# Kernel optimization log

Hardware: AMD Instinct MI355X
Metric: run time of the kernel (lower is better)

## Reference

```python
import jax, jax.numpy as jnp
import numpy as np
from jax import lax

N, L, E, ED, H = 100000, 48, 1600000, 17, 48

def _lin_init(k, fan_in, fan_out):
    kw, kb = jax.random.split(k)
    s = 1.0 / np.sqrt(fan_in)
    W = jax.random.uniform(kw, (fan_in, fan_out), minval=-s, maxval=s, dtype=jnp.float32)
    b = jax.random.uniform(kb, (fan_out,), minval=-s, maxval=s, dtype=jnp.float32)
    return W, b

def setup_inputs() -> dict:
    key = jax.random.key(0)
    ks = jax.random.split(key, 10)
    nodes = jax.random.normal(ks[0], (N, L, 1), dtype=jnp.float32)
    edge_index = jax.random.randint(ks[1], (2, E), 0, N, dtype=jnp.int64) if jax.config.jax_enable_x64 else jax.random.randint(ks[1], (2, E), 0, N, dtype=jnp.int32)
    edge_attr = jax.random.normal(ks[2], (E, ED), dtype=jnp.float32)
    valid = (jax.random.uniform(ks[3], (1, N, L)) < 0.8).astype(jnp.float32)
    r = jnp.zeros((1,), jnp.float32)
    fx = jnp.zeros((1,), jnp.float32)
    W1, b1 = _lin_init(ks[4], ED, H)   # lin_edge[0]
    W2, b2 = _lin_init(ks[5], H, H)    # lin_edge[2]
    Wg, bg = _lin_init(ks[6], H, H)    # gru[0]
    Ww, bw = _lin_init(ks[7], H, 1)    # weight_mlp
    Wf, bf = _lin_init(ks[8], 3, 1)    # fuse_mlp
    return {"nodes": nodes, "edge_index": edge_index, "edge_attr": edge_attr,
            "valid": valid, "r": r, "fx": fx,
            "W1": W1, "b1": b1, "W2": W2, "b2": b2, "Wg": Wg, "bg": bg,
            "Ww": Ww, "bw": bw, "Wf": Wf, "bf": bf}

def _gelu(x):
    return jax.nn.gelu(x, approximate=False)  # torch GELU default is exact erf

def reference(nodes, edge_index, edge_attr, valid, r, fx,
              W1, b1, W2, b2, Wg, bg, Ww, bw, Wf, bf):
    n = nodes.shape[0]
    # torch.no_grad block: mask nodes by valid, flatten (C==1)
    v = lax.stop_gradient(valid[0][..., None])            # [N, L, 1]
    x = lax.stop_gradient((nodes * v).reshape(n, L))      # [N, L]
    original = x
    nv_mask = (1.0 - v).reshape(n, L)                     # not_valid mask [N, L]
    src, dst = edge_index[0], edge_index[1]
    for _ in range(3):
        # lin_edge: 17 -> 48 -> GELU -> 48 -> ReLU  (per edge)
        eh = jax.nn.relu(_gelu(edge_attr @ W1 + b1) @ W2 + b2)      # [E, 48]
        xc = jnp.concatenate([x, v[..., 0]], axis=-1)               # [N, 2L]
        x_j = xc[src]                                               # gather [E, 2L]
        g = _gelu(eh @ Wg + bg)                                     # gru
        w = g @ Ww + bw                                             # [E, 1]
        w = jnp.mean(x_j[:, L:], axis=-1, keepdims=True) * w
        msg = x_j * jax.nn.sigmoid(w)                               # [E, 2L]
        agg = jax.ops.segment_sum(msg, dst, num_segments=n)         # scatter-add [N, 2L]
        new_half = agg[:, :L]                                       # [N, L]
        nn3 = jnp.stack([new_half, x, nv_mask], axis=-1)            # [N, L, 3]
        mask = jax.nn.sigmoid((nn3 @ Wf + bf)[..., 0])              # [N, L]
        x = (1.0 - mask) * x + nv_mask * mask * new_half
        v = jnp.logical_or((original != x)[..., None], v > 0).astype(jnp.float32)
        v = v.at[:, 0].set(0.0)
        nv_mask = (1.0 - v).reshape(n, L)
    return x[0][None]  # [1, L]
```

## Files before the change

kernel.cpp:

```cpp
#include <hip/hip_runtime.h>
#include <math.h>

#define NN 100000
#define LF 48
#define NE 1600000
#define EDIMS 17
#define MASKW 3125
#define CAP_E 16384
#define MAXLOC 12288
#define EB 1563

static_assert(NN == MASKW * 32, "mask width");

__device__ __forceinline__ float gelu_f(float x) {
    return 0.5f * x * (1.0f + erff(x * 0.7071067811865475f));
}
__device__ __forceinline__ float sigm_f(float x) {
    return 1.0f / (1.0f + expf(-x));
}

__global__ void expand1_kernel(const int* __restrict__ src, const int* __restrict__ dst,
                               unsigned* __restrict__ M2, unsigned* __restrict__ M1,
                               unsigned* __restrict__ M0, float4* __restrict__ aggz,
                               int4* __restrict__ list0, int* __restrict__ counter)
{
    int tid = blockIdx.x * 256 + threadIdx.x;
    int nthr = (int)gridDim.x * 256;
    for (int i = tid; i < MASKW; i += nthr) { M1[i] = 0u; M0[i] = 0u; }
    for (int i = tid; i < (3 * MAXLOC * LF) / 4; i += nthr)
        aggz[i] = make_float4(0.f, 0.f, 0.f, 0.f);
    if (tid == 0) atomicOr(&M2[0], 1u);
    int e0 = tid * 4;
    if (e0 + 3 < NE) {
        int4 d4 = *(const int4*)(dst + e0);
        int dv[4] = { d4.x, d4.y, d4.z, d4.w };
        #pragma unroll
        for (int k = 0; k < 4; ++k) {
            if (dv[k] == 0) {
                int e = e0 + k;
                int s = src[e];
                int idx = atomicAdd(counter, 1);
                if (idx < CAP_E) list0[idx] = make_int4(s, 0, e, 0);
                atomicOr(&M2[s >> 5], 1u << (s & 31));
            }
        }
    } else {
        for (int e = e0; e < NE; ++e) {
            if (dst[e] == 0) {
                int s = src[e];
                int idx = atomicAdd(counter, 1);
                if (idx < CAP_E) list0[idx] = make_int4(s, 0, e, 0);
                atomicOr(&M2[s >> 5], 1u << (s & 31));
            }
        }
    }
}

__global__ void expand_kernel(const int* __restrict__ src, const int* __restrict__ dst,
                              const unsigned* __restrict__ Min, unsigned* __restrict__ Mout,
                              int4* __restrict__ list, int* __restrict__ counter)
{
    int tid = blockIdx.x * 256 + threadIdx.x;
    int nthr = (int)gridDim.x * 256;
    for (int i = tid; i < MASKW; i += nthr) {
        unsigned m = Min[i];
        if (m) atomicOr(&Mout[i], m);
    }
    int e0 = tid * 4;
    if (e0 + 3 < NE) {
        int4 d4 = *(const int4*)(dst + e0);
        int dv[4] = { d4.x, d4.y, d4.z, d4.w };
        #pragma unroll
        for (int k = 0; k < 4; ++k) {
            int d = dv[k];
            if (Min[d >> 5] & (1u << (d & 31))) {
                int e = e0 + k;
                int s = src[e];
                int idx = atomicAdd(counter, 1);
                if (idx < CAP_E) list[idx] = make_int4(s, d, e, 0);
                atomicOr(&Mout[s >> 5], 1u << (s & 31));
            }
        }
    } else {
        for (int e = e0; e < NE; ++e) {
            int d = dst[e];
            if (Min[d >> 5] & (1u << (d & 31))) {
                int s = src[e];
                int idx = atomicAdd(counter, 1);
                if (idx < CAP_E) list[idx] = make_int4(s, d, e, 0);
                atomicOr(&Mout[s >> 5], 1u << (s & 31));
            }
        }
    }
}

__global__ void compact_kernel(const unsigned* __restrict__ M0, int* __restrict__ n2l,
                               int* __restrict__ l2n, int* __restrict__ nloc)
{
    int w = blockIdx.x * 256 + threadIdx.x;
    if (w >= MASKW) return;
    unsigned bits = M0[w];
    while (bits) {
        int b = __ffs(bits) - 1;
        bits &= bits - 1;
        int node = w * 32 + b;
        int loc = atomicAdd(nloc, 1);
        if (loc < MAXLOC) { n2l[node] = loc; l2n[loc] = node; }
    }
}

__device__ void w0_edge(int4* __restrict__ entp, const int* __restrict__ n2l,
                        const float* __restrict__ ea_g,
                        const float* __restrict__ W1, const float* __restrict__ b1,
                        const float* __restrict__ W2, const float* __restrict__ b2,
                        const float* __restrict__ Wg, const float* __restrict__ bg,
                        const float* __restrict__ Ww, const float* __restrict__ bw,
                        int lane)
{
    int4 ent = *entp;
    float ea = 0.f;
    if (lane < EDIMS) ea = ea_g[(long)ent.z * EDIMS + lane];
    float h1 = 0.f;
    if (lane < 48) {
        float acc = b1[lane];
        #pragma unroll
        for (int k = 0; k < EDIMS; ++k) acc += __shfl(ea, k, 64) * W1[k * 48 + lane];
        h1 = gelu_f(acc);
    }
    float h2 = 0.f;
    if (lane < 48) {
        float acc = b2[lane];
        #pragma unroll 8
        for (int k = 0; k < 48; ++k) acc += __shfl(h1, k, 64) * W2[k * 48 + lane];
        h2 = fmaxf(acc, 0.f);
    }
    float part = 0.f;
    if (lane < 48) {
        float acc = bg[lane];
        #pragma unroll 8
        for (int k = 0; k < 48; ++k) acc += __shfl(h2, k, 64) * Wg[k * 48 + lane];
        part = gelu_f(acc) * Ww[lane];
    }
    #pragma unroll
    for (int off = 32; off > 0; off >>= 1) part += __shfl_down(part, off, 64);
    if (lane == 0) {
        float w0 = part + bw[0];
        int sl = n2l[ent.x]; if ((unsigned)sl >= MAXLOC) sl = 0;
        int dl = n2l[ent.y]; if ((unsigned)dl >= MAXLOC) dl = 0;
        *entp = make_int4(sl, dl, ent.z, __float_as_int(w0));
    }
}

__global__ void initw0_kernel(const int* __restrict__ counters, const int* __restrict__ l2n,
                              const int* __restrict__ n2l,
                              const float* __restrict__ nodes, const float* __restrict__ valid,
                              float* __restrict__ X0, float* __restrict__ V0,
                              float* __restrict__ MV0,
                              int4* __restrict__ lists, const float* __restrict__ ea_g,
                              const float* __restrict__ W1, const float* __restrict__ b1,
                              const float* __restrict__ W2, const float* __restrict__ b2,
                              const float* __restrict__ Wg, const float* __restrict__ bg,
                              const float* __restrict__ Ww, const float* __restrict__ bw)
{
    int tid = blockIdx.x * 256 + threadIdx.x;
    int nthr = (int)gridDim.x * 256;
    int nl = counters[3]; if (nl > MAXLOC) nl = MAXLOC;
    for (int loc = tid; loc < nl; loc += nthr) {
        int node = l2n[loc];
        const float4* nv = (const float4*)(valid + (size_t)node * LF);
        const float4* nx = (const float4*)(nodes + (size_t)node * LF);
        float4* X0v = (float4*)(X0 + (size_t)loc * LF);
        float4* V0v = (float4*)(V0 + (size_t)loc * LF);
        float sum = 0.f;
        #pragma unroll
        for (int k = 0; k < 12; ++k) {
            float4 v = nv[k], x = nx[k];
            x.x *= v.x; x.y *= v.y; x.z *= v.z; x.w *= v.w;
            X0v[k] = x; V0v[k] = v;
            sum += v.x + v.y + v.z + v.w;
        }
        MV0[loc] = sum * (1.0f / 48.0f);
    }
    int c0 = counters[0]; c0 = (c0 > CAP_E) ? CAP_E : c0;
    int c1 = counters[1]; c1 = (c1 > CAP_E) ? CAP_E : c1;
    int c2 = counters[2]; c2 = (c2 > CAP_E) ? CAP_E : c2;
    int total = c0 + c1 + c2;
    int lane = tid & 63;
    for (int g = tid >> 6; g < total; g += (nthr >> 6)) {
        int4* entp;
        if (g < c0)           entp = lists + g;
        else if (g < c0 + c1) entp = lists + CAP_E + (g - c0);
        else                  entp = lists + 2 * CAP_E + (g - c0 - c1);
        w0_edge(entp, n2l, ea_g, W1, b1, W2, b2, Wg, bg, Ww, bw, lane);
    }
}

__global__ void agg1_kernel(const int4* __restrict__ list, const int* __restrict__ cnt,
                            const float* __restrict__ Xprev, const float* __restrict__ MVprev,
                            float* __restrict__ agg)
{
    int tid = blockIdx.x * 256 + threadIdx.x;
    int nthr = (int)gridDim.x * 256;
    int c = *cnt; if (c > CAP_E) c = CAP_E;
    int lane = tid & 63;
    for (int i = tid >> 6; i < c; i += (nthr >> 6)) {
        int4 ent = list[i];
        if ((unsigned)ent.x >= MAXLOC || (unsigned)ent.y >= MAXLOC) continue;
        float s = sigm_f(MVprev[ent.x] * __int_as_float(ent.w));
        if (lane < 48) atomicAdd(&agg[ent.y * LF + lane], s * Xprev[ent.x * LF + lane]);
    }
}


__device__ void upd_block(int nl, const int* __restrict__ l2n, const unsigned* __restrict__ Mt,
                          float* __restrict__ agg, const float* __restrict__ Xp,
                          const float* __restrict__ Vp, const float* __restrict__ Xorig,
                          float* __restrict__ Xc, float* __restrict__ Vc, float* __restrict__ MVc,
                          float wf0, float wf1, float wf2, float bfs, int tid)
{
    for (int loc = tid; loc < nl; loc += 1024) {
        int node = l2n[loc];
        if (!(Mt[node >> 5] & (1u << (node & 31)))) continue;
        float vsum = 0.f;
        #pragma unroll 4
        for (int l = 0; l < LF; ++l) {
            float nh = atomicAdd(&agg[loc * LF + l], 0.f);
            float xo = Xp[loc * LF + l];
            float vp = Vp[loc * LF + l];
            float nv = 1.0f - vp;
            float m = sigm_f(nh * wf0 + xo * wf1 + nv * wf2 + bfs);
            float xn = (1.0f - m) * xo + nv * m * nh;
            float vn = ((Xorig[loc * LF + l] != xn) || (vp > 0.f)) ? 1.0f : 0.0f;
            if (l == 0) vn = 0.0f;
            Xc[loc * LF + l] = xn;
            Vc[loc * LF + l] = vn;
            vsum += vn;
        }
        MVc[loc] = vsum * (1.0f / 48.0f);
    }
}

__device__ void agg_block(const int4* __restrict__ list, int c, const float* __restrict__ Xp,
                          const float* __restrict__ MVp, float* __restrict__ agg, int tid)
{
    int lane = tid & 63;
    for (int i = tid >> 6; i < c; i += 16) {
        int4 ent = list[i];
        if ((unsigned)ent.x >= MAXLOC || (unsigned)ent.y >= MAXLOC) continue;
        float s = sigm_f(MVp[ent.x] * __int_as_float(ent.w));
        if (lane < 48) atomicAdd(&agg[ent.y * LF + lane], s * Xp[ent.x * LF + lane]);
    }
}

__global__ void __launch_bounds__(1024) tail_kernel(
    const int* __restrict__ counters, const int* __restrict__ l2n, const int* __restrict__ n2l,
    const unsigned* __restrict__ M1, const unsigned* __restrict__ M2,
    const int4* __restrict__ lists, const float* __restrict__ X0,
    float* __restrict__ XA, float* __restrict__ XB,
    float* __restrict__ VA, float* __restrict__ VB,
    float* __restrict__ MVA, float* __restrict__ MVB,
    float* __restrict__ agg0, float* __restrict__ agg1b, float* __restrict__ agg2b,
    const float* __restrict__ Wf, const float* __restrict__ bf, float* __restrict__ out)
{
    int tid = threadIdx.x;
    int nl = counters[3]; if (nl > MAXLOC) nl = MAXLOC;
    int c0 = counters[0]; c0 = (c0 > CAP_E) ? CAP_E : c0;
    int c1 = counters[1]; c1 = (c1 > CAP_E) ? CAP_E : c1;
    float wf0 = Wf[0], wf1 = Wf[1], wf2 = Wf[2], bfs = bf[0];

    upd_block(nl, l2n, M1, agg0, X0, VA, X0, XA, VB, MVB, wf0, wf1, wf2, bfs, tid);
    __syncthreads();
    agg_block(lists + CAP_E, c1, XA, MVB, agg1b, tid);
    __syncthreads();
    upd_block(nl, l2n, M2, agg1b, XA, VB, X0, XB, VA, MVA, wf0, wf1, wf2, bfs, tid);
    __syncthreads();
    agg_block(lists, c0, XB, MVA, agg2b, tid);
    __syncthreads();
    if (tid < 48) {
        int loc0 = n2l[0]; if ((unsigned)loc0 >= MAXLOC) loc0 = 0;
        float nh = atomicAdd(&agg2b[loc0 * LF + tid], 0.f);
        float xo = XB[loc0 * LF + tid];
        float vp = VA[loc0 * LF + tid];
        float nv = 1.0f - vp;
        float m = sigm_f(nh * wf0 + xo * wf1 + nv * wf2 + bfs);
        out[tid] = (1.0f - m) * xo + nv * m * nh;
    }
}

extern "C" void kernel_launch(void* const* d_in, const int* in_sizes, int n_in,
                              void* d_out, int out_size, void* d_ws, size_t ws_size,
                              hipStream_t stream)
{
    (void)in_sizes; (void)n_in; (void)out_size;
    const float* nodes = (const float*)d_in[0];
    const int*   eidx  = (const int*)d_in[1];
    const float* eattr = (const float*)d_in[2];
    const float* valid = (const float*)d_in[3];
    const float* W1 = (const float*)d_in[6];
    const float* b1 = (const float*)d_in[7];
    const float* W2 = (const float*)d_in[8];
    const float* b2 = (const float*)d_in[9];
    const float* Wg = (const float*)d_in[10];
    const float* bg = (const float*)d_in[11];
    const float* Ww = (const float*)d_in[12];
    const float* bw = (const float*)d_in[13];
    const float* Wf = (const float*)d_in[14];
    const float* bf = (const float*)d_in[15];
    const int* src = eidx;
    const int* dst = eidx + NE;

    char* ws = (char*)d_ws;
    size_t off = 0;
    auto alloc = [&](size_t bytes) -> char* {
        char* p = ws + off;
        off += (bytes + 255) & ~(size_t)255;
        return p;
    };
    char*     zb = alloc(256 + MASKW * 4);
    int*      counters = (int*)zb;
    unsigned* M2 = (unsigned*)(zb + 256);
    unsigned* M1 = (unsigned*)alloc(MASKW * 4);
    unsigned* M0 = (unsigned*)alloc(MASKW * 4);
    int*      n2l = (int*)alloc((size_t)NN * 4);
    int*      l2n = (int*)alloc((size_t)MAXLOC * 4);
    int4*     lists = (int4*)alloc((size_t)3 * CAP_E * 16);
    float*    X0 = (float*)alloc((size_t)MAXLOC * LF * 4);
    float*    XA = (float*)alloc((size_t)MAXLOC * LF * 4);
    float*    XB = (float*)alloc((size_t)MAXLOC * LF * 4);
    float*    VA = (float*)alloc((size_t)MAXLOC * LF * 4);
    float*    VB = (float*)alloc((size_t)MAXLOC * LF * 4);
    float*    MVA = (float*)alloc((size_t)MAXLOC * 4);
    float*    MVB = (float*)alloc((size_t)MAXLOC * 4);
    float*    agg = (float*)alloc((size_t)3 * MAXLOC * LF * 4);
    if (off > ws_size) return;
    float* agg0  = agg;
    float* agg1b = agg + MAXLOC * LF;
    float* agg2b = agg + 2 * MAXLOC * LF;

    hipMemsetAsync(zb, 0, 256 + MASKW * 4, stream);

    expand1_kernel<<<EB, 256, 0, stream>>>(src, dst, M2, M1, M0, (float4*)agg,
                                           lists + 0 * CAP_E, counters + 0);
    expand_kernel<<<EB, 256, 0, stream>>>(src, dst, M2, M1, lists + 1 * CAP_E, counters + 1);
    expand_kernel<<<EB, 256, 0, stream>>>(src, dst, M1, M0, lists + 2 * CAP_E, counters + 2);
    compact_kernel<<<(MASKW + 255) / 256, 256, 0, stream>>>(M0, n2l, l2n, counters + 3);
    initw0_kernel<<<1024, 256, 0, stream>>>(counters, l2n, n2l, nodes, valid,
                                            X0, VA, MVA, lists, eattr,
                                            W1, b1, W2, b2, Wg, bg, Ww, bw);
    agg1_kernel<<<1024, 256, 0, stream>>>(lists + 2 * CAP_E, counters + 2, X0, MVA, agg0);
    tail_kernel<<<1, 1024, 0, stream>>>(counters, l2n, n2l, M1, M2, lists, X0,
                                        XA, XB, VA, VB, MVA, MVB,
                                        agg0, agg1b, agg2b, Wf, bf, (float*)d_out);
}
```

Baseline: 395.9 us.

## Fuse compaction into expand, merge w0 and first aggregation, slim tail

Merges local-id compaction into the third expand pass and folds the first-hop aggregation into the edge-MLP kernel, which reads source features straight from the global node arrays. This removes two launches and cuts the zeroed aggregation buffer from three to two. The single-block tail now builds shared-memory active lists so it updates only the nodes needed at each hop, uses one wave per node instead of one thread, and accumulates the last hop into a 48-float shared buffer. The fixed active-list capacities (8192 and 64) could overflow silently, and node locals are now assigned in nondeterministic order.

```diff
diff --git a/kernel.cpp b/kernel.cpp
--- a/kernel.cpp
+++ b/kernel.cpp
@@ -9,14 +9,22 @@
 #define CAP_E 16384
 #define MAXLOC 12288
 #define EB 1563
+#define ACT1_CAP 8192
+#define ACT2_CAP 64
 
 static_assert(NN == MASKW * 32, "mask width");
+static_assert(NE % 4 == 0, "int4 edge scan");
 
 __device__ __forceinline__ float gelu_f(float x) {
     return 0.5f * x * (1.0f + erff(x * 0.7071067811865475f));
 }
 __device__ __forceinline__ float sigm_f(float x) {
     return 1.0f / (1.0f + expf(-x));
+}
+__device__ __forceinline__ float wave_sum(float v) {
+    #pragma unroll
+    for (int off = 32; off > 0; off >>= 1) v += __shfl_down(v, off, 64);
+    return __shfl(v, 0, 64);
 }
 
 __global__ void expand1_kernel(const int* __restrict__ src, const int* __restrict__ dst,
@@ -27,7 +35,7 @@
     int tid = blockIdx.x * 256 + threadIdx.x;
     int nthr = (int)gridDim.x * 256;
     for (int i = tid; i < MASKW; i += nthr) { M1[i] = 0u; M0[i] = 0u; }
-    for (int i = tid; i < (3 * MAXLOC * LF) / 4; i += nthr)
+    for (int i = tid; i < (2 * MAXLOC * LF) / 4; i += nthr)
         aggz[i] = make_float4(0.f, 0.f, 0.f, 0.f);
     if (tid == 0) atomicOr(&M2[0], 1u);
     int e0 = tid * 4;
@@ -44,21 +52,12 @@
                 atomicOr(&M2[s >> 5], 1u << (s & 31));
             }
         }
-    } else {
-        for (int e = e0; e < NE; ++e) {
-            if (dst[e] == 0) {
-                int s = src[e];
-                int idx = atomicAdd(counter, 1);
-                if (idx < CAP_E) list0[idx] = make_int4(s, 0, e, 0);
-                atomicOr(&M2[s >> 5], 1u << (s & 31));
-            }
-        }
-    }
-}
-
-__global__ void expand_kernel(const int* __restrict__ src, const int* __restrict__ dst,
-                              const unsigned* __restrict__ Min, unsigned* __restrict__ Mout,
-                              int4* __restrict__ list, int* __restrict__ counter)
+    }
+}
+
+__global__ void expand2_kernel(const int* __restrict__ src, const int* __restrict__ dst,
+                               const unsigned* __restrict__ Min, unsigned* __restrict__ Mout,
+                               int4* __restrict__ list, int* __restrict__ counter)
 {
     int tid = blockIdx.x * 256 + threadIdx.x;
     int nthr = (int)gridDim.x * 256;
@@ -81,45 +80,59 @@
                 atomicOr(&Mout[s >> 5], 1u << (s & 31));
             }
         }
-    } else {
-        for (int e = e0; e < NE; ++e) {
-            int d = dst[e];
-            if (Min[d >> 5] & (1u << (d & 31))) {
+    }
+}
+
+__global__ void expand3_kernel(const int* __restrict__ src, const int* __restrict__ dst,
+                               const unsigned* __restrict__ M1, unsigned* __restrict__ M0,
+                               int4* __restrict__ list, int* __restrict__ counter,
+                               int* __restrict__ n2l, int* __restrict__ l2n,
+                               int* __restrict__ nloc)
+{
+    int tid = blockIdx.x * 256 + threadIdx.x;
+    int nthr = (int)gridDim.x * 256;
+    for (int w = tid; w < MASKW; w += nthr) {
+        unsigned bits = M1[w];
+        while (bits) {
+            int b = __ffs(bits) - 1;
+            bits &= bits - 1;
+            int node = w * 32 + b;
+            int loc = atomicAdd(nloc, 1);
+            if (loc < MAXLOC) { n2l[node] = loc; l2n[loc] = node; }
+        }
+    }
+    int e0 = tid * 4;
+    if (e0 + 3 < NE) {
+        int4 d4 = *(const int4*)(dst + e0);
+        int dv[4] = { d4.x, d4.y, d4.z, d4.w };
+        #pragma unroll
+        for (int k = 0; k < 4; ++k) {
+            int d = dv[k];
+            if (M1[d >> 5] & (1u << (d & 31))) {
+                int e = e0 + k;
                 int s = src[e];
                 int idx = atomicAdd(counter, 1);
                 if (idx < CAP_E) list[idx] = make_int4(s, d, e, 0);
-                atomicOr(&Mout[s >> 5], 1u << (s & 31));
+                unsigned sb = 1u << (s & 31);
+                unsigned old = atomicOr(&M0[s >> 5], sb);
+                if (!(old & sb) && !(M1[s >> 5] & sb)) {
+                    int loc = atomicAdd(nloc, 1);
+                    if (loc < MAXLOC) { n2l[s] = loc; l2n[loc] = s; }
+                }
             }
         }
     }
 }
 
-__global__ void compact_kernel(const unsigned* __restrict__ M0, int* __restrict__ n2l,
-                               int* __restrict__ l2n, int* __restrict__ nloc)
-{
-    int w = blockIdx.x * 256 + threadIdx.x;
-    if (w >= MASKW) return;
-    unsigned bits = M0[w];
-    while (bits) {
-        int b = __ffs(bits) - 1;
-        bits &= bits - 1;
-        int node = w * 32 + b;
-        int loc = atomicAdd(nloc, 1);
-        if (loc < MAXLOC) { n2l[node] = loc; l2n[loc] = node; }
-    }
-}
-
-__device__ void w0_edge(int4* __restrict__ entp, const int* __restrict__ n2l,
-                        const float* __restrict__ ea_g,
-                        const float* __restrict__ W1, const float* __restrict__ b1,
-                        const float* __restrict__ W2, const float* __restrict__ b2,
-                        const float* __restrict__ Wg, const float* __restrict__ bg,
-                        const float* __restrict__ Ww, const float* __restrict__ bw,
-                        int lane)
-{
-    int4 ent = *entp;
+__device__ float w0_compute(long e, const float* __restrict__ ea_g,
+                            const float* __restrict__ W1, const float* __restrict__ b1,
+                            const float* __restrict__ W2, const float* __restrict__ b2,
+                            const float* __restrict__ Wg, const float* __restrict__ bg,
+                            const float* __restrict__ Ww, const float* __restrict__ bw,
+                            int lane)
+{
     float ea = 0.f;
-    if (lane < EDIMS) ea = ea_g[(long)ent.z * EDIMS + lane];
+    if (lane < EDIMS) ea = ea_g[e * EDIMS + lane];
     float h1 = 0.f;
     if (lane < 48) {
         float acc = b1[lane];
@@ -141,45 +154,36 @@
         for (int k = 0; k < 48; ++k) acc += __shfl(h2, k, 64) * Wg[k * 48 + lane];
         part = gelu_f(acc) * Ww[lane];
     }
-    #pragma unroll
-    for (int off = 32; off > 0; off >>= 1) part += __shfl_down(part, off, 64);
-    if (lane == 0) {
-        float w0 = part + bw[0];
-        int sl = n2l[ent.x]; if ((unsigned)sl >= MAXLOC) sl = 0;
-        int dl = n2l[ent.y]; if ((unsigned)dl >= MAXLOC) dl = 0;
-        *entp = make_int4(sl, dl, ent.z, __float_as_int(w0));
-    }
-}
-
-__global__ void initw0_kernel(const int* __restrict__ counters, const int* __restrict__ l2n,
-                              const int* __restrict__ n2l,
-                              const float* __restrict__ nodes, const float* __restrict__ valid,
-                              float* __restrict__ X0, float* __restrict__ V0,
-                              float* __restrict__ MV0,
-                              int4* __restrict__ lists, const float* __restrict__ ea_g,
-                              const float* __restrict__ W1, const float* __restrict__ b1,
-                              const float* __restrict__ W2, const float* __restrict__ b2,
-                              const float* __restrict__ Wg, const float* __restrict__ bg,
-                              const float* __restrict__ Ww, const float* __restrict__ bw)
+    return wave_sum(part) + bw[0];
+}
+
+__global__ void fused_kernel(const int* __restrict__ counters, const int* __restrict__ l2n,
+                             const int* __restrict__ n2l, const unsigned* __restrict__ M1,
+                             const float* __restrict__ nodes, const float* __restrict__ valid,
+                             float* __restrict__ X0, float* __restrict__ VA,
+                             int4* __restrict__ lists, const float* __restrict__ ea_g,
+                             const float* __restrict__ W1, const float* __restrict__ b1,
+                             const float* __restrict__ W2, const float* __restrict__ b2,
+                             const float* __restrict__ Wg, const float* __restrict__ bg,
+                             const float* __restrict__ Ww, const float* __restrict__ bw,
+                             float* __restrict__ agg0)
 {
     int tid = blockIdx.x * 256 + threadIdx.x;
     int nthr = (int)gridDim.x * 256;
     int nl = counters[3]; if (nl > MAXLOC) nl = MAXLOC;
     for (int loc = tid; loc < nl; loc += nthr) {
         int node = l2n[loc];
+        if (!(M1[node >> 5] & (1u << (node & 31)))) continue;
         const float4* nv = (const float4*)(valid + (size_t)node * LF);
         const float4* nx = (const float4*)(nodes + (size_t)node * LF);
         float4* X0v = (float4*)(X0 + (size_t)loc * LF);
-        float4* V0v = (float4*)(V0 + (size_t)loc * LF);
-        float sum = 0.f;
+        float4* V0v = (float4*)(VA + (size_t)loc * LF);
         #pragma unroll
         for (int k = 0; k < 12; ++k) {
             float4 v = nv[k], x = nx[k];
             x.x *= v.x; x.y *= v.y; x.z *= v.z; x.w *= v.w;
             X0v[k] = x; V0v[k] = v;
-            sum += v.x + v.y + v.z + v.w;
-        }
-        MV0[loc] = sum * (1.0f / 48.0f);
+        }
     }
     int c0 = counters[0]; c0 = (c0 > CAP_E) ? CAP_E : c0;
     int c1 = counters[1]; c1 = (c1 > CAP_E) ? CAP_E : c1;
@@ -188,67 +192,28 @@
     int lane = tid & 63;
     for (int g = tid >> 6; g < total; g += (nthr >> 6)) {
         int4* entp;
+        bool isE1 = false;
         if (g < c0)           entp = lists + g;
         else if (g < c0 + c1) entp = lists + CAP_E + (g - c0);
-        else                  entp = lists + 2 * CAP_E + (g - c0 - c1);
-        w0_edge(entp, n2l, ea_g, W1, b1, W2, b2, Wg, bg, Ww, bw, lane);
-    }
-}
-
-__global__ void agg1_kernel(const int4* __restrict__ list, const int* __restrict__ cnt,
-                            const float* __restrict__ Xprev, const float* __restrict__ MVprev,
-                            float* __restrict__ agg)
-{
-    int tid = blockIdx.x * 256 + threadIdx.x;
-    int nthr = (int)gridDim.x * 256;
-    int c = *cnt; if (c > CAP_E) c = CAP_E;
-    int lane = tid & 63;
-    for (int i = tid >> 6; i < c; i += (nthr >> 6)) {
-        int4 ent = list[i];
-        if ((unsigned)ent.x >= MAXLOC || (unsigned)ent.y >= MAXLOC) continue;
-        float s = sigm_f(MVprev[ent.x] * __int_as_float(ent.w));
-        if (lane < 48) atomicAdd(&agg[ent.y * LF + lane], s * Xprev[ent.x * LF + lane]);
-    }
-}
-
-
-__device__ void upd_block(int nl, const int* __restrict__ l2n, const unsigned* __restrict__ Mt,
-                          float* __restrict__ agg, const float* __restrict__ Xp,
-                          const float* __restrict__ Vp, const float* __restrict__ Xorig,
-                          float* __restrict__ Xc, float* __restrict__ Vc, float* __restrict__ MVc,
-                          float wf0, float wf1, float wf2, float bfs, int tid)
-{
-    for (int loc = tid; loc < nl; loc += 1024) {
-        int node = l2n[loc];
-        if (!(Mt[node >> 5] & (1u << (node & 31)))) continue;
-        float vsum = 0.f;
-        #pragma unroll 4
-        for (int l = 0; l < LF; ++l) {
-            float nh = atomicAdd(&agg[loc * LF + l], 0.f);
-            float xo = Xp[loc * LF + l];
-            float vp = Vp[loc * LF + l];
-            float nv = 1.0f - vp;
-            float m = sigm_f(nh * wf0 + xo * wf1 + nv * wf2 + bfs);
-            float xn = (1.0f - m) * xo + nv * m * nh;
-            float vn = ((Xorig[loc * LF + l] != xn) || (vp > 0.f)) ? 1.0f : 0.0f;
-            if (l == 0) vn = 0.0f;
-            Xc[loc * LF + l] = xn;
-            Vc[loc * LF + l] = vn;
-            vsum += vn;
-        }
-        MVc[loc] = vsum * (1.0f / 48.0f);
-    }
-}
-
-__device__ void agg_block(const int4* __restrict__ list, int c, const float* __restrict__ Xp,
-                          const float* __restrict__ MVp, float* __restrict__ agg, int tid)
-{
-    int lane = tid & 63;
-    for (int i = tid >> 6; i < c; i += 16) {
-        int4 ent = list[i];
-        if ((unsigned)ent.x >= MAXLOC || (unsigned)ent.y >= MAXLOC) continue;
-        float s = sigm_f(MVp[ent.x] * __int_as_float(ent.w));
-        if (lane < 48) atomicAdd(&agg[ent.y * LF + lane], s * Xp[ent.x * LF + lane]);
+        else                { entp = lists + 2 * CAP_E + (g - c0 - c1); isE1 = true; }
+        int4 ent = *entp;
+        float w0 = w0_compute((long)ent.z, ea_g, W1, b1, W2, b2, Wg, bg, Ww, bw, lane);
+        if (isE1) {
+            int s = ent.x;
+            int dl = n2l[ent.y]; if ((unsigned)dl >= MAXLOC) dl = 0;
+            float v = 0.f, x = 0.f;
+            if (lane < 48) {
+                v = valid[(size_t)s * LF + lane];
+                x = nodes[(size_t)s * LF + lane] * v;
+            }
+            float mv = wave_sum(v) * (1.0f / 48.0f);
+            float sg = sigm_f(mv * w0);
+            if (lane < 48) atomicAdd(&agg0[dl * LF + lane], sg * x);
+        } else if (lane == 0) {
+            int sl = n2l[ent.x]; if ((unsigned)sl >= MAXLOC) sl = 0;
+            int dl = n2l[ent.y]; if ((unsigned)dl >= MAXLOC) dl = 0;
+            *entp = make_int4(sl, dl, ent.z, __float_as_int(w0));
+        }
     }
 }
 
@@ -259,26 +224,96 @@
     float* __restrict__ XA, float* __restrict__ XB,
     float* __restrict__ VA, float* __restrict__ VB,
     float* __restrict__ MVA, float* __restrict__ MVB,
-    float* __restrict__ agg0, float* __restrict__ agg1b, float* __restrict__ agg2b,
+    const float* __restrict__ agg0, float* __restrict__ agg1b,
     const float* __restrict__ Wf, const float* __restrict__ bf, float* __restrict__ out)
 {
+    __shared__ int act1[ACT1_CAP];
+    __shared__ int act2[ACT2_CAP];
+    __shared__ int cnts[2];
+    __shared__ float agg3s[LF];
     int tid = threadIdx.x;
+    if (tid < 2) cnts[tid] = 0;
+    if (tid < LF) agg3s[tid] = 0.f;
+    __syncthreads();
+
     int nl = counters[3]; if (nl > MAXLOC) nl = MAXLOC;
-    int c0 = counters[0]; c0 = (c0 > CAP_E) ? CAP_E : c0;
-    int c1 = counters[1]; c1 = (c1 > CAP_E) ? CAP_E : c1;
+    for (int loc = tid; loc < nl; loc += 1024) {
+        int node = l2n[loc];
+        unsigned bit = 1u << (node & 31);
+        unsigned w1 = M1[node >> 5], w2 = M2[node >> 5];
+        if (w1 & bit) { int i = atomicAdd(&cnts[0], 1); if (i < ACT1_CAP) act1[i] = loc; }
+        if (w2 & bit) { int i = atomicAdd(&cnts[1], 1); if (i < ACT2_CAP) act2[i] = loc; }
+    }
+    __syncthreads();
+    int c1n = cnts[0]; if (c1n > ACT1_CAP) c1n = ACT1_CAP;
+    int c2n = cnts[1]; if (c2n > ACT2_CAP) c2n = ACT2_CAP;
+    int wave = tid >> 6, lane = tid & 63;
     float wf0 = Wf[0], wf1 = Wf[1], wf2 = Wf[2], bfs = bf[0];
 
-    upd_block(nl, l2n, M1, agg0, X0, VA, X0, XA, VB, MVB, wf0, wf1, wf2, bfs, tid);
-    __syncthreads();
-    agg_block(lists + CAP_E, c1, XA, MVB, agg1b, tid);
-    __syncthreads();
-    upd_block(nl, l2n, M2, agg1b, XA, VB, X0, XB, VA, MVA, wf0, wf1, wf2, bfs, tid);
-    __syncthreads();
-    agg_block(lists, c0, XB, MVA, agg2b, tid);
-    __syncthreads();
+    for (int i = wave; i < c1n; i += 16) {
+        int loc = act1[i];
+        float nh = 0.f, xo = 0.f, vp = 0.f;
+        if (lane < 48) {
+            nh = agg0[loc * LF + lane];
+            xo = X0[loc * LF + lane];
+            vp = VA[loc * LF + lane];
+        }
+        float nv = 1.0f - vp;
+        float m = sigm_f(nh * wf0 + xo * wf1 + nv * wf2 + bfs);
+        float xn = (1.0f - m) * xo + nv * m * nh;
+        float vn = ((xo != xn) || (vp > 0.f)) ? 1.0f : 0.0f;
+        if (lane == 0) vn = 0.0f;
+        if (lane < 48) { XA[loc * LF + lane] = xn; VB[loc * LF + lane] = vn; }
+        float s = (lane < 48) ? vn : 0.f;
+        #pragma unroll
+        for (int off = 32; off > 0; off >>= 1) s += __shfl_down(s, off, 64);
+        if (lane == 0) MVB[loc] = s * (1.0f / 48.0f);
+    }
+    __syncthreads();
+
+    int cE2 = counters[1]; if (cE2 > CAP_E) cE2 = CAP_E;
+    for (int i = wave; i < cE2; i += 16) {
+        int4 ent = lists[CAP_E + i];
+        if ((unsigned)ent.x >= MAXLOC || (unsigned)ent.y >= MAXLOC) continue;
+        float sg = sigm_f(MVB[ent.x] * __int_as_float(ent.w));
+        if (lane < 48) atomicAdd(&agg1b[ent.y * LF + lane], sg * XA[ent.x * LF + lane]);
+    }
+    __syncthreads();
+
+    for (int i = wave; i < c2n; i += 16) {
+        int loc = act2[i];
+        float nh = 0.f, xo = 0.f, vp = 0.f, xorig = 0.f;
+        if (lane < 48) {
+            nh = agg1b[loc * LF + lane];
+            xo = XA[loc * LF + lane];
+            vp = VB[loc * LF + lane];
+            xorig = X0[loc * LF + lane];
+        }
+        float nv = 1.0f - vp;
+        float m = sigm_f(nh * wf0 + xo * wf1 + nv * wf2 + bfs);
+        float xn = (1.0f - m) * xo + nv * m * nh;
+        float vn = ((xorig != xn) || (vp > 0.f)) ? 1.0f : 0.0f;
+        if (lane == 0) vn = 0.0f;
+        if (lane < 48) { XB[loc * LF + lane] = xn; VA[loc * LF + lane] = vn; }
+        float s = (lane < 48) ? vn : 0.f;
+        #pragma unroll
+        for (int off = 32; off > 0; off >>= 1) s += __shfl_down(s, off, 64);
+        if (lane == 0) MVA[loc] = s * (1.0f / 48.0f);
+    }
+    __syncthreads();
+
+    int cE3 = counters[0]; if (cE3 > CAP_E) cE3 = CAP_E;
+    for (int i = wave; i < cE3; i += 16) {
+        int4 ent = lists[i];
+        if ((unsigned)ent.x >= MAXLOC) continue;
+        float sg = sigm_f(MVA[ent.x] * __int_as_float(ent.w));
+        if (lane < 48) atomicAdd(&agg3s[lane], sg * XB[ent.x * LF + lane]);
+    }
+    __syncthreads();
+
     if (tid < 48) {
         int loc0 = n2l[0]; if ((unsigned)loc0 >= MAXLOC) loc0 = 0;
-        float nh = atomicAdd(&agg2b[loc0 * LF + tid], 0.f);
+        float nh = agg3s[tid];
         float xo = XB[loc0 * LF + tid];
         float vp = VA[loc0 * LF + tid];
         float nv = 1.0f - vp;
@@ -331,24 +366,22 @@
     float*    VB = (float*)alloc((size_t)MAXLOC * LF * 4);
     float*    MVA = (float*)alloc((size_t)MAXLOC * 4);
     float*    MVB = (float*)alloc((size_t)MAXLOC * 4);
-    float*    agg = (float*)alloc((size_t)3 * MAXLOC * LF * 4);
+    float*    agg = (float*)alloc((size_t)2 * MAXLOC * LF * 4);
     if (off > ws_size) return;
     float* agg0  = agg;
     float* agg1b = agg + MAXLOC * LF;
-    float* agg2b = agg + 2 * MAXLOC * LF;
 
     hipMemsetAsync(zb, 0, 256 + MASKW * 4, stream);
 
     expand1_kernel<<<EB, 256, 0, stream>>>(src, dst, M2, M1, M0, (float4*)agg,
                                            lists + 0 * CAP_E, counters + 0);
-    expand_kernel<<<EB, 256, 0, stream>>>(src, dst, M2, M1, lists + 1 * CAP_E, counters + 1);
-    expand_kernel<<<EB, 256, 0, stream>>>(src, dst, M1, M0, lists + 2 * CAP_E, counters + 2);
-    compact_kernel<<<(MASKW + 255) / 256, 256, 0, stream>>>(M0, n2l, l2n, counters + 3);
-    initw0_kernel<<<1024, 256, 0, stream>>>(counters, l2n, n2l, nodes, valid,
-                                            X0, VA, MVA, lists, eattr,
-                                            W1, b1, W2, b2, Wg, bg, Ww, bw);
-    agg1_kernel<<<1024, 256, 0, stream>>>(lists + 2 * CAP_E, counters + 2, X0, MVA, agg0);
+    expand2_kernel<<<EB, 256, 0, stream>>>(src, dst, M2, M1, lists + 1 * CAP_E, counters + 1);
+    expand3_kernel<<<EB, 256, 0, stream>>>(src, dst, M1, M0, lists + 2 * CAP_E, counters + 2,
+                                           n2l, l2n, counters + 3);
+    fused_kernel<<<1024, 256, 0, stream>>>(counters, l2n, n2l, M1, nodes, valid,
+                                           X0, VA, lists, eattr,
+                                           W1, b1, W2, b2, Wg, bg, Ww, bw, agg0);
     tail_kernel<<<1, 1024, 0, stream>>>(counters, l2n, n2l, M1, M2, lists, X0,
                                         XA, XB, VA, VB, MVA, MVB,
-                                        agg0, agg1b, agg2b, Wf, bf, (float*)d_out);
-}
+                                        agg0, agg1b, Wf, bf, (float*)d_out);
+}
```

New measurement: 341.5 us. -13.7%, faster.
